# Kernel optimization log

Measured on AMD Instinct MI355X. Metric: run time of the kernel, lower is better.

Reference implementation:

```python
import jax, jax.numpy as jnp
import numpy as np

B, N, D = 2, 2048, 1024
H, DH = 16, 64
DI = 4096
EPS = 1e-5
NEG_SLOPE = 0.01  # F.leaky_relu default


def _ln(x, g, b):
    mu = jnp.mean(x, axis=-1, keepdims=True)
    var = jnp.mean((x - mu) ** 2, axis=-1, keepdims=True)
    return (x - mu) * jax.lax.rsqrt(var + EPS) * g + b


def setup_inputs() -> dict:
    key = jax.random.key(0)
    ks = jax.random.split(key, 10)
    s = 0.02
    return {
        "Z": jax.random.normal(ks[0], (B, N, D), jnp.float32),
        "new_mask": jax.random.normal(ks[1], (B, N, N), jnp.float32),
        "mask": jax.random.uniform(ks[2], (B, N, N), jnp.float32),
        "ln1_g": jnp.ones((D,), jnp.float32),
        "ln1_b": jnp.zeros((D,), jnp.float32),
        "qkv_w": jax.random.normal(ks[3], (3 * D, D), jnp.float32) * s,
        "qkv_b": jnp.zeros((3 * D,), jnp.float32),
        "o_w": jax.random.normal(ks[4], (D, H * DH), jnp.float32) * s,
        "ln2_g": jnp.ones((D,), jnp.float32),
        "ln2_b": jnp.zeros((D,), jnp.float32),
        "p1_w": jax.random.normal(ks[5], (DI, D), jnp.float32) * s,
        "p1_b": jnp.zeros((DI,), jnp.float32),
        "p2_w": jax.random.normal(ks[6], (D, DI), jnp.float32) * s,
        "p2_b": jnp.zeros((D,), jnp.float32),
    }


def reference(Z, new_mask, mask, ln1_g, ln1_b, qkv_w, qkv_b, o_w, ln2_g, ln2_b, p1_w, p1_b, p2_w, p2_b):
    inp = Z
    Zn = _ln(Z, ln1_g, ln1_b)
    qkv = (Zn @ qkv_w.T + qkv_b).reshape(B, N, H, 3 * DH)
    # torch chunk order in the source: V, Q, K
    V, Q, K = jnp.split(qkv, 3, axis=3)  # each [B,N,H,DH]
    # scores: einsum('bnij,bmij->binm') == [B,H,N,N]
    W = jnp.einsum("bnhd,bmhd->bhnm", Q, K) / np.sqrt(DH) + new_mask[:, None]
    A = jax.nn.softmax(W, axis=3) * mask[:, None]
    attn = jnp.einsum("bhnm,bmhd->bnhd", A, V).reshape(B, N, D)
    attn = jnp.where(attn >= 0, attn, NEG_SLOPE * attn) @ o_w.T  # leaky_relu then o_net (no bias)
    Z1 = attn + inp
    Zn2 = _ln(Z1, ln2_g, ln2_b)
    h = jax.nn.relu(Zn2 @ p1_w.T + p1_b)
    return h @ p2_w.T + p2_b + Z1
```

## Files before the change

kernel.cpp:

```cpp
#include <hip/hip_runtime.h>

typedef unsigned short u16;
typedef __attribute__((ext_vector_type(8))) short bf16x8;
typedef __attribute__((ext_vector_type(2))) float f32x2;
typedef __attribute__((ext_vector_type(4))) float f32x4;
typedef __attribute__((ext_vector_type(16))) float f32x16;
typedef __attribute__((ext_vector_type(4))) unsigned u32x4;

#define DEV static __device__ __forceinline__

DEV u16 f2bf(float f) {
    unsigned u = __float_as_uint(f);
    u += 0x7FFFu + ((u >> 16) & 1u);
    return (u16)(u >> 16);
}

DEV float uaf(unsigned u) { return __uint_as_float(u); }

typedef const __attribute__((address_space(1))) void* gas1_t;
typedef __attribute__((address_space(3))) void* gas3_t;

DEV void gl_lds16(const u16* g, u16* l) {
    __builtin_amdgcn_global_load_lds((gas1_t)g, (gas3_t)l, 16, 0, 0);
}

DEV unsigned cvtpk_bf16(float a, float b) {
    unsigned r;
    asm("v_cvt_pk_bf16_f32 %0, %1, %2" : "=v"(r) : "v"(a), "v"(b));
    return r;
}

DEV int sw8(int row, int chunk) { return row * 64 + ((chunk ^ (row & 7)) << 3); }

__global__ __launch_bounds__(256) void prep_all(const float* __restrict__ qkv_w,
                                                const float* __restrict__ o_w,
                                                const float* __restrict__ p1_w,
                                                const float* __restrict__ p2_w,
                                                const float* __restrict__ qkv_b,
                                                const float* __restrict__ nm,
                                                const float* __restrict__ pm,
                                                u16* __restrict__ qkvW,
                                                u16* __restrict__ oW,
                                                u16* __restrict__ p1W,
                                                u16* __restrict__ p2W,
                                                float* __restrict__ pbias,
                                                unsigned* __restrict__ Mp) {
    const int bid = blockIdx.x, t = threadIdx.x;
    if (bid < 3072) {
        int i = bid * 256 + t;
        int orow = i >> 8, cc = i & 255;
        int region = orow >> 10, rem = orow & 1023, h = rem >> 6, tt = rem & 63;
        int srow = h * 192 + region * 64 + tt;
        float4 v = ((const float4*)qkv_w)[srow * 256 + cc];
        ushort4 o;
        o.x = f2bf(v.x); o.y = f2bf(v.y); o.z = f2bf(v.z); o.w = f2bf(v.w);
        ((ushort4*)qkvW)[i] = o;
    } else if (bid < 4096) {
        int i = (bid - 3072) * 256 + t;
        float4 v = ((const float4*)o_w)[i];
        ushort4 o;
        o.x = f2bf(v.x); o.y = f2bf(v.y); o.z = f2bf(v.z); o.w = f2bf(v.w);
        ((ushort4*)oW)[i] = o;
    } else if (bid < 8192) {
        int i = (bid - 4096) * 256 + t;
        float4 v = ((const float4*)p1_w)[i];
        ushort4 o;
        o.x = f2bf(v.x); o.y = f2bf(v.y); o.z = f2bf(v.z); o.w = f2bf(v.w);
        ((ushort4*)p1W)[i] = o;
    } else if (bid < 12288) {
        int i = (bid - 8192) * 256 + t;
        float4 v = ((const float4*)p2_w)[i];
        ushort4 o;
        o.x = f2bf(v.x); o.y = f2bf(v.y); o.z = f2bf(v.z); o.w = f2bf(v.w);
        ((ushort4*)p2W)[i] = o;
    } else if (bid < 20480) {
        int i = (bid - 12288) * 256 + t;
        float4 a = ((const float4*)nm)[i];
        float4 b = ((const float4*)pm)[i];
        uint4 o;
        o.x = ((unsigned)f2bf(b.x) << 16) | f2bf(a.x * 8.0f);
        o.y = ((unsigned)f2bf(b.y) << 16) | f2bf(a.y * 8.0f);
        o.z = ((unsigned)f2bf(b.z) << 16) | f2bf(a.z * 8.0f);
        o.w = ((unsigned)f2bf(b.w) << 16) | f2bf(a.w * 8.0f);
        int e = i * 4;
        int bb = e >> 22;
        int rem = e & 4194303;
        int n = rem >> 11;
        int m = rem & 2047;
        int mt = m >> 5;
        int m5 = m & 31;
        int c = m5 >> 3;
        int hi = (m5 >> 2) & 1;
        size_t oi = (((size_t)(bb * 64 + mt) * 4 + c) * 2048 + n) * 2 + hi;
        ((uint4*)Mp)[oi] = o;
    } else {
#pragma unroll
        for (int k = 0; k < 12; k++) {
            int i = k * 256 + t;
            int region = i >> 10, rem = i & 1023, h = rem >> 6, tt = rem & 63;
            pbias[i] = qkv_b[h * 192 + region * 64 + tt];
        }
    }
}

__global__ __launch_bounds__(256) void ln_bf16(const float* __restrict__ x,
                                               const float* __restrict__ gam,
                                               const float* __restrict__ bet,
                                               u16* __restrict__ y) {
    const int row = blockIdx.x;
    const int t = threadIdx.x;
    const float4 v = ((const float4*)(x + (size_t)row * 1024))[t];
    float s = v.x + v.y + v.z + v.w;
    float ss = v.x * v.x + v.y * v.y + v.z * v.z + v.w * v.w;
#pragma unroll
    for (int o = 1; o < 64; o <<= 1) {
        s += __shfl_xor(s, o);
        ss += __shfl_xor(ss, o);
    }
    __shared__ float rs[4], rss[4];
    const int wave = t >> 6, lane = t & 63;
    if (lane == 0) { rs[wave] = s; rss[wave] = ss; }
    __syncthreads();
    const float tot = rs[0] + rs[1] + rs[2] + rs[3];
    const float totss = rss[0] + rss[1] + rss[2] + rss[3];
    const float mu = tot * (1.0f / 1024.0f);
    const float var = totss * (1.0f / 1024.0f) - mu * mu;
    const float rstd = rsqrtf(var + 1e-5f);
    const float4 g4 = ((const float4*)gam)[t];
    const float4 b4 = ((const float4*)bet)[t];
    ushort4 o;
    o.x = f2bf((v.x - mu) * rstd * g4.x + b4.x);
    o.y = f2bf((v.y - mu) * rstd * g4.y + b4.y);
    o.z = f2bf((v.z - mu) * rstd * g4.z + b4.z);
    o.w = f2bf((v.w - mu) * rstd * g4.w + b4.w);
    ((ushort4*)(y + (size_t)row * 1024))[t] = o;
}

__global__ __launch_bounds__(256) void ln2_comb4(const float* __restrict__ p0,
                                                 const float* __restrict__ p1,
                                                 const float* __restrict__ p2,
                                                 const float* __restrict__ p3,
                                                 const float* __restrict__ Z,
                                                 const float* __restrict__ gam,
                                                 const float* __restrict__ bet,
                                                 float* __restrict__ Z1,
                                                 u16* __restrict__ y) {
    const int row = blockIdx.x;
    const int t = threadIdx.x;
    const size_t off = (size_t)row * 256 + t;
    const float4 a = ((const float4*)p0)[off];
    const float4 c = ((const float4*)p1)[off];
    const float4 d = ((const float4*)p2)[off];
    const float4 e = ((const float4*)p3)[off];
    const float4 z = ((const float4*)Z)[off];
    float4 v;
    v.x = a.x + c.x + d.x + e.x + z.x;
    v.y = a.y + c.y + d.y + e.y + z.y;
    v.z = a.z + c.z + d.z + e.z + z.z;
    v.w = a.w + c.w + d.w + e.w + z.w;
    ((float4*)Z1)[off] = v;
    float s = v.x + v.y + v.z + v.w;
    float ss = v.x * v.x + v.y * v.y + v.z * v.z + v.w * v.w;
#pragma unroll
    for (int o = 1; o < 64; o <<= 1) {
        s += __shfl_xor(s, o);
        ss += __shfl_xor(ss, o);
    }
    __shared__ float rs[4], rss[4];
    const int wave = t >> 6, lane = t & 63;
    if (lane == 0) { rs[wave] = s; rss[wave] = ss; }
    __syncthreads();
    const float tot = rs[0] + rs[1] + rs[2] + rs[3];
    const float totss = rss[0] + rss[1] + rss[2] + rss[3];
    const float mu = tot * (1.0f / 1024.0f);
    const float var = totss * (1.0f / 1024.0f) - mu * mu;
    const float rstd = rsqrtf(var + 1e-5f);
    const float4 g4 = ((const float4*)gam)[t];
    const float4 b4 = ((const float4*)bet)[t];
    ushort4 o;
    o.x = f2bf((v.x - mu) * rstd * g4.x + b4.x);
    o.y = f2bf((v.y - mu) * rstd * g4.y + b4.y);
    o.z = f2bf((v.z - mu) * rstd * g4.z + b4.z);
    o.w = f2bf((v.w - mu) * rstd * g4.w + b4.w);
    ((ushort4*)(y + (size_t)row * 1024))[t] = o;
}

__global__ __launch_bounds__(256) void out_comb(const float* __restrict__ p0,
                                                const float* __restrict__ p1,
                                                const float* __restrict__ bias,
                                                const float* __restrict__ Z1,
                                                float* __restrict__ out) {
    int i = blockIdx.x * 256 + threadIdx.x;
    float4 a = ((const float4*)p0)[i];
    float4 c = ((const float4*)p1)[i];
    float4 z = ((const float4*)Z1)[i];
    float4 b = ((const float4*)bias)[i & 255];
    float4 o;
    o.x = a.x + c.x + z.x + b.x; o.y = a.y + c.y + z.y + b.y;
    o.z = a.z + c.z + z.z + b.z; o.w = a.w + c.w + z.w + b.w;
    ((float4*)out)[i] = o;
}

template <int EPI>
__global__ __launch_bounds__(256, 3) void gemm_bt(const u16* __restrict__ A,
                                                  const u16* __restrict__ Bt,
                                                  const float* __restrict__ bias,
                                                  void* __restrict__ out0,
                                                  void* __restrict__ out1,
                                                  void* __restrict__ out2,
                                                  int M, int N, int K, int ldk) {
    __shared__ __align__(16) u16 As[128 * 32];
    __shared__ __align__(16) u16 Bs[128 * 32];
    const int tid = threadIdx.x;
    const int wave = tid >> 6, lane = tid & 63;
    const int lhi = lane >> 4, llo = lane & 15;
    const int bx = blockIdx.x, by = blockIdx.y;
    const int kz = blockIdx.z * K;

    const int arow = wave * 32 + (lane >> 2);
    const int acol = (lane & 3) * 8;
    const u16* gA = A + (size_t)(by * 128 + arow) * ldk + kz + acol;
    const u16* gB = Bt + (size_t)(bx * 128 + arow) * ldk + kz + acol;
    u16* lA = As + wave * 1024 + lane * 8;
    u16* lB = Bs + wave * 1024 + lane * 8;

    const int wr = wave >> 1, wc = wave & 1;
    const f32x4 zero = {0.f, 0.f, 0.f, 0.f};
    f32x4 acc[4][4];
#pragma unroll
    for (int i = 0; i < 4; i++)
#pragma unroll
        for (int j = 0; j < 4; j++) acc[i][j] = zero;

    for (int k0 = 0; k0 < K; k0 += 32) {
        __syncthreads();
        gl_lds16(gA, lA);
        gl_lds16(gA + 16 * (size_t)ldk, lA + 512);
        gl_lds16(gB, lB);
        gl_lds16(gB + 16 * (size_t)ldk, lB + 512);
        gA += 32; gB += 32;
        __syncthreads();
        bf16x8 af[4], bfr[4];
#pragma unroll
        for (int i = 0; i < 4; i++)
            af[i] = *(const bf16x8*)(As + (wr * 64 + i * 16 + llo) * 32 + lhi * 8);
#pragma unroll
        for (int j = 0; j < 4; j++)
            bfr[j] = *(const bf16x8*)(Bs + (wc * 64 + j * 16 + llo) * 32 + lhi * 8);
#pragma unroll
        for (int i = 0; i < 4; i++)
#pragma unroll
            for (int j = 0; j < 4; j++)
                acc[i][j] = __builtin_amdgcn_mfma_f32_16x16x32_bf16(af[i], bfr[j], acc[i][j], 0, 0, 0);
    }

    const int rbase = by * 128 + wr * 64 + lhi * 4;
    const int cbase = bx * 128 + wc * 64 + llo;
    if constexpr (EPI == 0) {
        if (cbase < 1024) {
#pragma unroll
            for (int i = 0; i < 4; i++) {
                const int row0 = rbase + i * 16;
                const int bb = row0 >> 11, nn = row0 & 2047;
                const int g5 = (nn >> 2) & 7;
                const int pg = (g5 & 4) | ((g5 & 1) << 1) | ((g5 >> 1) & 1);
                const int nnp = (nn & ~31) | (pg << 2);
#pragma unroll
                for (int j = 0; j < 4; j++) {
                    const int col = cbase + j * 16;
                    const float bv = bias[col];
                    const int h = col >> 6, d = col & 63;
                    ushort4 o4;
                    o4.x = f2bf(acc[i][j][0] + bv);
                    o4.y = f2bf(acc[i][j][1] + bv);
                    o4.z = f2bf(acc[i][j][2] + bv);
                    o4.w = f2bf(acc[i][j][3] + bv);
                    *(ushort4*)((u16*)out0 + ((size_t)(bb * 16 + h) * 64 + d) * 2048 + nnp) = o4;
                }
            }
        } else {
#pragma unroll
            for (int i = 0; i < 4; i++) {
#pragma unroll
                for (int j = 0; j < 4; j++) {
#pragma unroll
                    for (int r = 0; r < 4; r++) {
                        const int row = rbase + i * 16 + r;
                        const int col = cbase + j * 16;
                        float v = acc[i][j][r] + bias[col];
                        const int region = col >> 10;
                        const int c = col & 1023;
                        const int b = row >> 11, n = row & 2047;
                        const int h = c >> 6, t = c & 63;
                        u16* dst = (region == 1) ? (u16*)out1 : (u16*)out2;
                        dst[(((size_t)(b * 16 + h)) * 2048 + n) * 64 + t] = f2bf(v);
                    }
                }
            }
        }
    } else {
        float* pout = nullptr;
        if constexpr (EPI == 4) {
            pout = (blockIdx.z < 2) ? ((float*)out0 + (size_t)blockIdx.z * M * N)
                                    : ((float*)out1 + (size_t)(blockIdx.z - 2) * M * N);
        }
#pragma unroll
        for (int i = 0; i < 4; i++) {
#pragma unroll
            for (int j = 0; j < 4; j++) {
#pragma unroll
                for (int r = 0; r < 4; r++) {
                    const int row = rbase + i * 16 + r;
                    const int col = cbase + j * 16;
                    float v = acc[i][j][r];
                    if constexpr (EPI == 2) {
                        v += bias[col];
                        v = v > 0.f ? v : 0.f;
                        ((u16*)out0)[(size_t)row * N + col] = f2bf(v);
                    } else {
                        pout[(size_t)row * N + col] = v;
                    }
                }
            }
        }
    }
}

__global__ __launch_bounds__(256, 4) void attn_fused7(const u16* __restrict__ Qg,
                                                      const u16* __restrict__ Kg,
                                                      const u16* __restrict__ Vtg,
                                                      const unsigned* __restrict__ Mp,
                                                      u16* __restrict__ attnL) {
    __shared__ __align__(16) u16 Ks[2][64 * 64];
    __shared__ __align__(16) u16 Vs[2][64 * 64];
    __shared__ float lsh[2][32], lsh2[2][32];
    const int tid = threadIdx.x, wave = tid >> 6, lane = tid & 63;
    const int qh = wave & 1, wm = wave >> 1;
    const int hi = lane >> 5, l31 = lane & 31;
    const int pid = blockIdx.x;
    const int seq = pid >> 3;
    const int hh = seq & 15;
    const int g = (pid & 7) + (seq >> 4) * 8;
    const int b = g >> 5, qt = g & 31;
    const int bh = b * 16 + hh;
    const int q0 = qt * 64;

    const int l3 = lane >> 3, l7 = lane & 7;
    const int swcol = (l7 ^ l3) << 3;
    const int srow = wave * 16 + l3;
    const u16* kp = Kg + ((size_t)bh * 2048 + srow) * 64 + swcol;
    const u16* vp = Vtg + ((size_t)bh * 64 + srow) * 2048 + swcol;
    u16* lKa = Ks[0] + wave * 1024 + lane * 8;
    u16* lKb = Ks[1] + wave * 1024 + lane * 8;
    u16* lVa = Vs[0] + wave * 1024 + lane * 8;
    u16* lVb = Vs[1] + wave * 1024 + lane * 8;

#define STAGE(LK, LV) do { \
        gl_lds16(kp, LK); gl_lds16(kp + 512, (LK) + 512); \
        gl_lds16(vp, LV); gl_lds16(vp + 16384, (LV) + 512); \
        kp += 4096; vp += 64; } while (0)

    STAGE(lKa, lVa);
    const int qrow = q0 + qh * 32 + l31;
    const u16* qptr = Qg + ((size_t)bh * 2048 + qrow) * 64 + hi * 8;
    bf16x8 qf[4];
#pragma unroll
    for (int ks = 0; ks < 4; ks++) qf[ks] = *(const bf16x8*)(qptr + ks * 16);

    const uint4* mb4 = (const uint4*)Mp + ((size_t)(b * 64 + wm) * 4) * 4096
                                        + (size_t)qrow * 2 + hi;
    uint4 mA0 = mb4[0], mA1 = mb4[4096], mA2 = mb4[8192], mA3 = mb4[12288];
    uint4 mB0, mB1, mB2, mB3;
    const uint4* mn = mb4 + 32768;

    const f32x16 z16 = {0.f,0.f,0.f,0.f,0.f,0.f,0.f,0.f,0.f,0.f,0.f,0.f,0.f,0.f,0.f,0.f};
    f32x16 accO[2];
    accO[0] = z16; accO[1] = z16;
    f32x2 lsv = {0.f, 0.f};
    const float CS = 0.125f * 1.4426950f;
    __syncthreads();

#define QUAD(M, q) { \
        f32x2 s0 = {sacc[q] * CS, sacc[q + 1] * CS}; \
        f32x2 s1 = {sacc[q + 2] * CS, sacc[q + 3] * CS}; \
        f32x2 e0 = {__builtin_amdgcn_exp2f(s0.x), __builtin_amdgcn_exp2f(s0.y)}; \
        f32x2 e1 = {__builtin_amdgcn_exp2f(s1.x), __builtin_amdgcn_exp2f(s1.y)}; \
        lsv += e0; lsv += e1; \
        f32x2 pm0 = {uaf(M.x & 0xFFFF0000u), uaf(M.y & 0xFFFF0000u)}; \
        f32x2 pm1 = {uaf(M.z & 0xFFFF0000u), uaf(M.w & 0xFFFF0000u)}; \
        e0 *= pm0; e1 *= pm1; \
        wpk[(q) / 2] = cvtpk_bf16(e0.x, e0.y); \
        wpk[(q) / 2 + 1] = cvtpk_bf16(e1.x, e1.y); }

#define ITER(KSB, VSB, M0, M1, M2, M3) do { \
        f32x16 sacc; \
        sacc[0] = uaf(M0.x << 16); sacc[1] = uaf(M0.y << 16); \
        sacc[2] = uaf(M0.z << 16); sacc[3] = uaf(M0.w << 16); \
        sacc[4] = uaf(M1.x << 16); sacc[5] = uaf(M1.y << 16); \
        sacc[6] = uaf(M1.z << 16); sacc[7] = uaf(M1.w << 16); \
        sacc[8] = uaf(M2.x << 16); sacc[9] = uaf(M2.y << 16); \
        sacc[10] = uaf(M2.z << 16); sacc[11] = uaf(M2.w << 16); \
        sacc[12] = uaf(M3.x << 16); sacc[13] = uaf(M3.y << 16); \
        sacc[14] = uaf(M3.z << 16); sacc[15] = uaf(M3.w << 16); \
        __builtin_amdgcn_s_setprio(1); \
        _Pragma("unroll") \
        for (int ks = 0; ks < 4; ks++) { \
            const bf16x8 kf = *(const bf16x8*)((KSB) + sw8(wm * 32 + l31, ks * 2 + hi)); \
            sacc = __builtin_amdgcn_mfma_f32_32x32x16_bf16(kf, qf[ks], sacc, 0, 0, 0); \
        } \
        __builtin_amdgcn_s_setprio(0); \
        unsigned wpk[8]; \
        QUAD(M0, 0) QUAD(M1, 4) QUAD(M2, 8) QUAD(M3, 12) \
        const u32x4 fa0v = {wpk[0], wpk[1], wpk[2], wpk[3]}; \
        const u32x4 fa1v = {wpk[4], wpk[5], wpk[6], wpk[7]}; \
        const bf16x8 pa0 = __builtin_bit_cast(bf16x8, fa0v); \
        const bf16x8 pa1 = __builtin_bit_cast(bf16x8, fa1v); \
        __builtin_amdgcn_s_setprio(1); \
        _Pragma("unroll") \
        for (int dh = 0; dh < 2; dh++) { \
            const bf16x8 vf0 = *(const bf16x8*)((VSB) + sw8(dh * 32 + l31, wm * 4 + hi)); \
            accO[dh] = __builtin_amdgcn_mfma_f32_32x32x16_bf16(pa0, vf0, accO[dh], 0, 0, 0); \
            const bf16x8 vf1 = *(const bf16x8*)((VSB) + sw8(dh * 32 + l31, wm * 4 + 2 + hi)); \
            accO[dh] = __builtin_amdgcn_mfma_f32_32x32x16_bf16(pa1, vf1, accO[dh], 0, 0, 0); \
        } \
        __builtin_amdgcn_s_setprio(0); \
        __syncthreads(); } while (0)

    for (int tt = 0; tt < 16; tt++) {
        mB0 = mn[0]; mB1 = mn[4096]; mB2 = mn[8192]; mB3 = mn[12288]; mn += 32768;
        STAGE(lKb, lVb);
        ITER(Ks[0], Vs[0], mA0, mA1, mA2, mA3);
        if (tt < 15) {
            mA0 = mn[0]; mA1 = mn[4096]; mA2 = mn[8192]; mA3 = mn[12288]; mn += 32768;
            STAGE(lKa, lVa);
        }
        ITER(Ks[1], Vs[1], mB0, mB1, mB2, mB3);
    }
#undef ITER
#undef QUAD
#undef STAGE

    const float lsum = lsv.x + lsv.y;
    const float lsum2 = lsum + __shfl_xor(lsum, 32);
    float* cb = (float*)&Ks[0][0];
    const int slot = qh * 64 + lane;
    const int s7 = slot & 7;
    if (wm == 1) {
        float* dst = cb + (size_t)slot * 32;
#pragma unroll
        for (int dh = 0; dh < 2; dh++)
#pragma unroll
            for (int c = 0; c < 4; c++) {
                const f32x4 v = {accO[dh][c * 4 + 0], accO[dh][c * 4 + 1],
                                 accO[dh][c * 4 + 2], accO[dh][c * 4 + 3]};
                *(f32x4*)(dst + (((dh * 4 + c) ^ s7) << 2)) = v;
            }
        if (lane < 32) lsh[qh][lane] = lsum2;
    }
    __syncthreads();
    if (wm == 0) {
        const float* src = cb + (size_t)slot * 32;
        const float lt = lsum2 + lsh[qh][l31];
#pragma unroll
        for (int dh = 0; dh < 2; dh++)
#pragma unroll
            for (int c = 0; c < 4; c++) {
                const f32x4 v = *(const f32x4*)(src + (((dh * 4 + c) ^ s7) << 2));
                accO[dh][c * 4 + 0] += v.x;
                accO[dh][c * 4 + 1] += v.y;
                accO[dh][c * 4 + 2] += v.z;
                accO[dh][c * 4 + 3] += v.w;
            }
        if (lane < 32) lsh2[qh][lane] = 1.0f / lt;
    }
    __syncthreads();
    if (wm == 0) {
#pragma unroll
        for (int r = 0; r < 16; r++) {
            const int ql = (r & 3) + 8 * (r >> 2) + 4 * hi;
            const float linv = lsh2[qh][ql];
            const int qg = q0 + qh * 32 + ql;
#pragma unroll
            for (int dh = 0; dh < 2; dh++) {
                float v = accO[dh][r] * linv;
                v = v >= 0.f ? v : 0.01f * v;
                attnL[((size_t)b * 2048 + qg) * 1024 + hh * 64 + dh * 32 + l31] = f2bf(v);
            }
        }
    }
}

extern "C" void kernel_launch(void* const* d_in, const int* in_sizes, int n_in,
                              void* d_out, int out_size, void* d_ws, size_t ws_size,
                              hipStream_t stream) {
    const float* Z     = (const float*)d_in[0];
    const float* nmask = (const float*)d_in[1];
    const float* pmask = (const float*)d_in[2];
    const float* ln1_g = (const float*)d_in[3];
    const float* ln1_b = (const float*)d_in[4];
    const float* qkv_w = (const float*)d_in[5];
    const float* qkv_b = (const float*)d_in[6];
    const float* o_w   = (const float*)d_in[7];
    const float* ln2_g = (const float*)d_in[8];
    const float* ln2_b = (const float*)d_in[9];
    const float* p1_w  = (const float*)d_in[10];
    const float* p1_b  = (const float*)d_in[11];
    const float* p2_w  = (const float*)d_in[12];
    const float* p2_b  = (const float*)d_in[13];
    float* out = (float*)d_out;

    char* w = (char*)d_ws;
    auto take = [&](size_t bytes) -> char* {
        char* p = w;
        w += (bytes + 255) & ~(size_t)255;
        return p;
    };
    u16* qkvW   = (u16*)take((size_t)3072 * 1024 * 2);
    u16* oW     = (u16*)take((size_t)1024 * 1024 * 2);
    u16* p1W    = (u16*)take((size_t)4096 * 1024 * 2);
    u16* p2W    = (u16*)take((size_t)1024 * 4096 * 2);
    u16* Zn     = (u16*)take((size_t)4096 * 1024 * 2);
    u16* Qb     = (u16*)take((size_t)32 * 2048 * 64 * 2);
    u16* Kb     = (u16*)take((size_t)32 * 2048 * 64 * 2);
    u16* Vt     = (u16*)take((size_t)32 * 64 * 2048 * 2);
    u16* attnL  = (u16*)take((size_t)4096 * 1024 * 2);
    float* Z1   = (float*)take((size_t)4096 * 1024 * 4);
    u16* hbuf   = (u16*)take((size_t)4096 * 4096 * 2);
    unsigned* Mp = (unsigned*)take((size_t)2 * 2048 * 2048 * 4);
    float* pbias = (float*)take((size_t)3072 * 4);
    float* part01 = (float*)Mp;
    float* part23 = (float*)hbuf;

    prep_all<<<dim3(20481), 256, 0, stream>>>(qkv_w, o_w, p1_w, p2_w, qkv_b, nmask, pmask,
                                              qkvW, oW, p1W, p2W, pbias, Mp);
    ln_bf16<<<dim3(4096), 256, 0, stream>>>(Z, ln1_g, ln1_b, Zn);
    gemm_bt<0><<<dim3(24, 32), 256, 0, stream>>>(Zn, qkvW, pbias, Vt, Qb, Kb, 4096, 3072, 1024, 1024);
    attn_fused7<<<dim3(1024), 256, 0, stream>>>(Qb, Kb, Vt, Mp, attnL);
    gemm_bt<4><<<dim3(8, 32, 4), 256, 0, stream>>>(attnL, oW, nullptr, part01, part23, nullptr,
                                                   4096, 1024, 256, 1024);
    ln2_comb4<<<dim3(4096), 256, 0, stream>>>(part01, part01 + (size_t)4096 * 1024,
                                              part23, part23 + (size_t)4096 * 1024,
                                              Z, ln2_g, ln2_b, Z1, Zn);
    gemm_bt<2><<<dim3(32, 32), 256, 0, stream>>>(Zn, p1W, p1_b, hbuf, nullptr, nullptr,
                                                 4096, 4096, 1024, 1024);
    gemm_bt<4><<<dim3(8, 32, 2), 256, 0, stream>>>(hbuf, p2W, nullptr, part01, nullptr, nullptr,
                                                   4096, 1024, 2048, 4096);
    out_comb<<<dim3(4096), 256, 0, stream>>>(part01, part01 + (size_t)4096 * 1024, p2_b, Z1, out);
}
```

Before: 467.7 us.

## Coalesce mask packing via LDS, split V transpose into kernel, restructure mask loads

After: 437.0 us. -6.6%, faster.

```diff
diff --git a/kernel.cpp b/kernel.cpp
--- a/kernel.cpp
+++ b/kernel.cpp
@@ -45,6 +45,7 @@
                                                 u16* __restrict__ p2W,
                                                 float* __restrict__ pbias,
                                                 unsigned* __restrict__ Mp) {
+    __shared__ uint4 Ls[512];
     const int bid = blockIdx.x, t = threadIdx.x;
     if (bid < 3072) {
         int i = bid * 256 + t;
@@ -73,26 +74,35 @@
         ushort4 o;
         o.x = f2bf(v.x); o.y = f2bf(v.y); o.z = f2bf(v.z); o.w = f2bf(v.w);
         ((ushort4*)p2W)[i] = o;
-    } else if (bid < 20480) {
-        int i = (bid - 12288) * 256 + t;
-        float4 a = ((const float4*)nm)[i];
-        float4 b = ((const float4*)pm)[i];
-        uint4 o;
-        o.x = ((unsigned)f2bf(b.x) << 16) | f2bf(a.x * 8.0f);
-        o.y = ((unsigned)f2bf(b.y) << 16) | f2bf(a.y * 8.0f);
-        o.z = ((unsigned)f2bf(b.z) << 16) | f2bf(a.z * 8.0f);
-        o.w = ((unsigned)f2bf(b.w) << 16) | f2bf(a.w * 8.0f);
-        int e = i * 4;
-        int bb = e >> 22;
-        int rem = e & 4194303;
-        int n = rem >> 11;
-        int m = rem & 2047;
-        int mt = m >> 5;
-        int m5 = m & 31;
-        int c = m5 >> 3;
-        int hi = (m5 >> 2) & 1;
-        size_t oi = (((size_t)(bb * 64 + mt) * 4 + c) * 2048 + n) * 2 + hi;
-        ((uint4*)Mp)[oi] = o;
+    } else if (bid < 16384) {
+        const int idx = bid - 12288;
+        const int bb = idx >> 11, r2 = idx & 2047;
+        const int mt = r2 >> 5, nt = r2 & 31;
+        const int n0 = nt * 64;
+        const int n = t >> 2;
+        const int mq0 = (t & 3) * 2;
+        const size_t fbase = (size_t)bb * 1048576 + (size_t)(n0 + n) * 512 + mt * 8 + mq0;
+        const float4 a0 = ((const float4*)nm)[fbase];
+        const float4 a1 = ((const float4*)nm)[fbase + 1];
+        const float4 b0 = ((const float4*)pm)[fbase];
+        const float4 b1 = ((const float4*)pm)[fbase + 1];
+        uint4 o0, o1;
+        o0.x = ((unsigned)f2bf(b0.x) << 16) | f2bf(a0.x * 1.4426950f);
+        o0.y = ((unsigned)f2bf(b0.y) << 16) | f2bf(a0.y * 1.4426950f);
+        o0.z = ((unsigned)f2bf(b0.z) << 16) | f2bf(a0.z * 1.4426950f);
+        o0.w = ((unsigned)f2bf(b0.w) << 16) | f2bf(a0.w * 1.4426950f);
+        o1.x = ((unsigned)f2bf(b1.x) << 16) | f2bf(a1.x * 1.4426950f);
+        o1.y = ((unsigned)f2bf(b1.y) << 16) | f2bf(a1.y * 1.4426950f);
+        o1.z = ((unsigned)f2bf(b1.z) << 16) | f2bf(a1.z * 1.4426950f);
+        o1.w = ((unsigned)f2bf(b1.w) << 16) | f2bf(a1.w * 1.4426950f);
+        const int c = mq0 >> 1;
+        Ls[c * 128 + n * 2 + 0] = o0;
+        Ls[c * 128 + n * 2 + 1] = o1;
+        __syncthreads();
+        const int wc = t >> 6, j = t & 63;
+        const size_t obase = (((size_t)(bb * 64 + mt) * 4) + wc) * 4096 + (size_t)n0 * 2;
+        ((uint4*)Mp)[obase + j] = Ls[wc * 128 + j];
+        ((uint4*)Mp)[obase + 64 + j] = Ls[wc * 128 + 64 + j];
     } else {
 #pragma unroll
         for (int k = 0; k < 12; k++) {
@@ -256,77 +266,81 @@
 
     const int rbase = by * 128 + wr * 64 + lhi * 4;
     const int cbase = bx * 128 + wc * 64 + llo;
-    if constexpr (EPI == 0) {
-        if (cbase < 1024) {
-#pragma unroll
-            for (int i = 0; i < 4; i++) {
-                const int row0 = rbase + i * 16;
-                const int bb = row0 >> 11, nn = row0 & 2047;
-                const int g5 = (nn >> 2) & 7;
-                const int pg = (g5 & 4) | ((g5 & 1) << 1) | ((g5 >> 1) & 1);
-                const int nnp = (nn & ~31) | (pg << 2);
-#pragma unroll
-                for (int j = 0; j < 4; j++) {
-                    const int col = cbase + j * 16;
-                    const float bv = bias[col];
-                    const int h = col >> 6, d = col & 63;
-                    ushort4 o4;
-                    o4.x = f2bf(acc[i][j][0] + bv);
-                    o4.y = f2bf(acc[i][j][1] + bv);
-                    o4.z = f2bf(acc[i][j][2] + bv);
-                    o4.w = f2bf(acc[i][j][3] + bv);
-                    *(ushort4*)((u16*)out0 + ((size_t)(bb * 16 + h) * 64 + d) * 2048 + nnp) = o4;
-                }
-            }
-        } else {
-#pragma unroll
-            for (int i = 0; i < 4; i++) {
-#pragma unroll
-                for (int j = 0; j < 4; j++) {
-#pragma unroll
-                    for (int r = 0; r < 4; r++) {
-                        const int row = rbase + i * 16 + r;
-                        const int col = cbase + j * 16;
-                        float v = acc[i][j][r] + bias[col];
-                        const int region = col >> 10;
-                        const int c = col & 1023;
-                        const int b = row >> 11, n = row & 2047;
+    float* pout = nullptr;
+    if constexpr (EPI == 4) {
+        pout = (blockIdx.z < 2) ? ((float*)out0 + (size_t)blockIdx.z * M * N)
+                                : ((float*)out1 + (size_t)(blockIdx.z - 2) * M * N);
+    }
+#pragma unroll
+    for (int i = 0; i < 4; i++) {
+#pragma unroll
+        for (int j = 0; j < 4; j++) {
+#pragma unroll
+            for (int r = 0; r < 4; r++) {
+                const int row = rbase + i * 16 + r;
+                const int col = cbase + j * 16;
+                float v = acc[i][j][r];
+                if constexpr (EPI == 0) {
+                    v += bias[col];
+                    const int region = col >> 10;
+                    const int c = col & 1023;
+                    const int b = row >> 11, n = row & 2047;
+                    if (region == 0) {
+                        ((float*)out0)[(size_t)row * 1024 + c] = v;
+                    } else {
                         const int h = c >> 6, t = c & 63;
                         u16* dst = (region == 1) ? (u16*)out1 : (u16*)out2;
                         dst[(((size_t)(b * 16 + h)) * 2048 + n) * 64 + t] = f2bf(v);
                     }
+                } else if constexpr (EPI == 2) {
+                    v += bias[col];
+                    v = v > 0.f ? v : 0.f;
+                    ((u16*)out0)[(size_t)row * N + col] = f2bf(v);
+                } else {
+                    pout[(size_t)row * N + col] = v;
                 }
             }
         }
-    } else {
-        float* pout = nullptr;
-        if constexpr (EPI == 4) {
-            pout = (blockIdx.z < 2) ? ((float*)out0 + (size_t)blockIdx.z * M * N)
-                                    : ((float*)out1 + (size_t)(blockIdx.z - 2) * M * N);
-        }
-#pragma unroll
-        for (int i = 0; i < 4; i++) {
-#pragma unroll
-            for (int j = 0; j < 4; j++) {
-#pragma unroll
-                for (int r = 0; r < 4; r++) {
-                    const int row = rbase + i * 16 + r;
-                    const int col = cbase + j * 16;
-                    float v = acc[i][j][r];
-                    if constexpr (EPI == 2) {
-                        v += bias[col];
-                        v = v > 0.f ? v : 0.f;
-                        ((u16*)out0)[(size_t)row * N + col] = f2bf(v);
-                    } else {
-                        pout[(size_t)row * N + col] = v;
-                    }
-                }
-            }
-        }
-    }
-}
-
-__global__ __launch_bounds__(256, 4) void attn_fused7(const u16* __restrict__ Qg,
+    }
+}
+
+__global__ __launch_bounds__(256) void vtrans(const float* __restrict__ Vsc,
+                                              u16* __restrict__ Vt) {
+    __shared__ u16 Ts[64 * 72];
+    const int nt = blockIdx.x;
+    const int bh = blockIdx.y;
+    const int b = bh >> 4, h = bh & 15;
+    const int t = threadIdx.x;
+    const int n0 = nt * 64;
+    const int nr = t >> 2;
+    const int dq = (t & 3) * 16;
+    const float* src = Vsc + ((size_t)(b * 2048 + n0 + nr)) * 1024 + h * 64 + dq;
+    float4 v0 = ((const float4*)src)[0];
+    float4 v1 = ((const float4*)src)[1];
+    float4 v2 = ((const float4*)src)[2];
+    float4 v3 = ((const float4*)src)[3];
+    u16* c0 = Ts + nr;
+    c0[(dq + 0) * 72]  = f2bf(v0.x); c0[(dq + 1) * 72]  = f2bf(v0.y);
+    c0[(dq + 2) * 72]  = f2bf(v0.z); c0[(dq + 3) * 72]  = f2bf(v0.w);
+    c0[(dq + 4) * 72]  = f2bf(v1.x); c0[(dq + 5) * 72]  = f2bf(v1.y);
+    c0[(dq + 6) * 72]  = f2bf(v1.z); c0[(dq + 7) * 72]  = f2bf(v1.w);
+    c0[(dq + 8) * 72]  = f2bf(v2.x); c0[(dq + 9) * 72]  = f2bf(v2.y);
+    c0[(dq + 10) * 72] = f2bf(v2.z); c0[(dq + 11) * 72] = f2bf(v2.w);
+    c0[(dq + 12) * 72] = f2bf(v3.x); c0[(dq + 13) * 72] = f2bf(v3.y);
+    c0[(dq + 14) * 72] = f2bf(v3.z); c0[(dq + 15) * 72] = f2bf(v3.w);
+    __syncthreads();
+    const int d = t >> 2, n8 = (t & 3) * 16;
+    u16* dstrow = Vt + ((size_t)bh * 64 + d) * 2048 + n0;
+#pragma unroll
+    for (int w = 0; w < 4; w++) {
+        const int gi = (n8 >> 2) + w;
+        const int g5 = gi & 7, blk = gi >> 3;
+        const int pg = (g5 & 4) | ((g5 & 1) << 1) | ((g5 >> 1) & 1);
+        *(uint2*)(dstrow + blk * 32 + pg * 4) = *(const uint2*)(Ts + d * 72 + n8 + w * 4);
+    }
+}
+
+__global__ __launch_bounds__(256, 4) void attn_fused8(const u16* __restrict__ Qg,
                                                       const u16* __restrict__ Kg,
                                                       const u16* __restrict__ Vtg,
                                                       const unsigned* __restrict__ Mp,
@@ -367,41 +381,37 @@
 #pragma unroll
     for (int ks = 0; ks < 4; ks++) qf[ks] = *(const bf16x8*)(qptr + ks * 16);
 
-    const uint4* mb4 = (const uint4*)Mp + ((size_t)(b * 64 + wm) * 4) * 4096
-                                        + (size_t)qrow * 2 + hi;
-    uint4 mA0 = mb4[0], mA1 = mb4[4096], mA2 = mb4[8192], mA3 = mb4[12288];
-    uint4 mB0, mB1, mB2, mB3;
-    const uint4* mn = mb4 + 32768;
+    const uint4* mp = (const uint4*)Mp + (size_t)(b * 64 + wm) * 16384
+                                       + (size_t)qrow * 2 + hi;
 
     const f32x16 z16 = {0.f,0.f,0.f,0.f,0.f,0.f,0.f,0.f,0.f,0.f,0.f,0.f,0.f,0.f,0.f,0.f};
     f32x16 accO[2];
     accO[0] = z16; accO[1] = z16;
     f32x2 lsv = {0.f, 0.f};
     const float CS = 0.125f * 1.4426950f;
+    const f32x2 csv = {CS, CS};
     __syncthreads();
 
 #define QUAD(M, q) { \
-        f32x2 s0 = {sacc[q] * CS, sacc[q + 1] * CS}; \
-        f32x2 s1 = {sacc[q + 2] * CS, sacc[q + 3] * CS}; \
-        f32x2 e0 = {__builtin_amdgcn_exp2f(s0.x), __builtin_amdgcn_exp2f(s0.y)}; \
-        f32x2 e1 = {__builtin_amdgcn_exp2f(s1.x), __builtin_amdgcn_exp2f(s1.y)}; \
+        f32x2 nm0 = {uaf(M.x << 16), uaf(M.y << 16)}; \
+        f32x2 nm1 = {uaf(M.z << 16), uaf(M.w << 16)}; \
+        const f32x2 sa = {sacc[q], sacc[q + 1]}; \
+        const f32x2 sb = {sacc[q + 2], sacc[q + 3]}; \
+        nm0 += sa * csv; nm1 += sb * csv; \
+        f32x2 e0 = {__builtin_amdgcn_exp2f(nm0.x), __builtin_amdgcn_exp2f(nm0.y)}; \
+        f32x2 e1 = {__builtin_amdgcn_exp2f(nm1.x), __builtin_amdgcn_exp2f(nm1.y)}; \
         lsv += e0; lsv += e1; \
-        f32x2 pm0 = {uaf(M.x & 0xFFFF0000u), uaf(M.y & 0xFFFF0000u)}; \
-        f32x2 pm1 = {uaf(M.z & 0xFFFF0000u), uaf(M.w & 0xFFFF0000u)}; \
+        const f32x2 pm0 = {uaf(M.x & 0xFFFF0000u), uaf(M.y & 0xFFFF0000u)}; \
+        const f32x2 pm1 = {uaf(M.z & 0xFFFF0000u), uaf(M.w & 0xFFFF0000u)}; \
         e0 *= pm0; e1 *= pm1; \
         wpk[(q) / 2] = cvtpk_bf16(e0.x, e0.y); \
         wpk[(q) / 2 + 1] = cvtpk_bf16(e1.x, e1.y); }
 
-#define ITER(KSB, VSB, M0, M1, M2, M3) do { \
-        f32x16 sacc; \
-        sacc[0] = uaf(M0.x << 16); sacc[1] = uaf(M0.y << 16); \
-        sacc[2] = uaf(M0.z << 16); sacc[3] = uaf(M0.w << 16); \
-        sacc[4] = uaf(M1.x << 16); sacc[5] = uaf(M1.y << 16); \
-        sacc[6] = uaf(M1.z << 16); sacc[7] = uaf(M1.w << 16); \
-        sacc[8] = uaf(M2.x << 16); sacc[9] = uaf(M2.y << 16); \
-        sacc[10] = uaf(M2.z << 16); sacc[11] = uaf(M2.w << 16); \
-        sacc[12] = uaf(M3.x << 16); sacc[13] = uaf(M3.y << 16); \
-        sacc[14] = uaf(M3.z << 16); sacc[15] = uaf(M3.w << 16); \
+#define ITER(KSB, VSB, LK, LV, DO_STAGE) do { \
+        const uint4 M0 = mp[0], M1 = mp[4096], M2 = mp[8192], M3 = mp[12288]; \
+        mp += 32768; \
+        if (DO_STAGE) STAGE(LK, LV); \
+        f32x16 sacc = z16; \
         __builtin_amdgcn_s_setprio(1); \
         _Pragma("unroll") \
         for (int ks = 0; ks < 4; ks++) { \
@@ -427,14 +437,8 @@
         __syncthreads(); } while (0)
 
     for (int tt = 0; tt < 16; tt++) {
-        mB0 = mn[0]; mB1 = mn[4096]; mB2 = mn[8192]; mB3 = mn[12288]; mn += 32768;
-        STAGE(lKb, lVb);
-        ITER(Ks[0], Vs[0], mA0, mA1, mA2, mA3);
-        if (tt < 15) {
-            mA0 = mn[0]; mA1 = mn[4096]; mA2 = mn[8192]; mA3 = mn[12288]; mn += 32768;
-            STAGE(lKa, lVa);
-        }
-        ITER(Ks[1], Vs[1], mB0, mB1, mB2, mB3);
+        ITER(Ks[0], Vs[0], lKb, lVb, true);
+        ITER(Ks[1], Vs[1], lKa, lVa, (tt < 15));
     }
 #undef ITER
 #undef QUAD
@@ -528,14 +532,16 @@
     u16* hbuf   = (u16*)take((size_t)4096 * 4096 * 2);
     unsigned* Mp = (unsigned*)take((size_t)2 * 2048 * 2048 * 4);
     float* pbias = (float*)take((size_t)3072 * 4);
+    float* Vsc    = (float*)hbuf;
     float* part01 = (float*)Mp;
     float* part23 = (float*)hbuf;
 
-    prep_all<<<dim3(20481), 256, 0, stream>>>(qkv_w, o_w, p1_w, p2_w, qkv_b, nmask, pmask,
+    prep_all<<<dim3(16385), 256, 0, stream>>>(qkv_w, o_w, p1_w, p2_w, qkv_b, nmask, pmask,
                                               qkvW, oW, p1W, p2W, pbias, Mp);
     ln_bf16<<<dim3(4096), 256, 0, stream>>>(Z, ln1_g, ln1_b, Zn);
-    gemm_bt<0><<<dim3(24, 32), 256, 0, stream>>>(Zn, qkvW, pbias, Vt, Qb, Kb, 4096, 3072, 1024, 1024);
-    attn_fused7<<<dim3(1024), 256, 0, stream>>>(Qb, Kb, Vt, Mp, attnL);
+    gemm_bt<0><<<dim3(24, 32), 256, 0, stream>>>(Zn, qkvW, pbias, Vsc, Qb, Kb, 4096, 3072, 1024, 1024);
+    vtrans<<<dim3(32, 32), 256, 0, stream>>>(Vsc, Vt);
+    attn_fused8<<<dim3(1024), 256, 0, stream>>>(Qb, Kb, Vt, Mp, attnL);
     gemm_bt<4><<<dim3(8, 32, 4), 256, 0, stream>>>(attnL, oW, nullptr, part01, part23, nullptr,
                                                    4096, 1024, 256, 1024);
     ln2_comb4<<<dim3(4096), 256, 0, stream>>>(part01, part01 + (size_t)4096 * 1024,
```
